# Performance work log

Hardware: AMD Instinct MI355X
Metric: run time of the kernel (lower is better)

Reference implementation:

```python
import jax, jax.numpy as jnp
import numpy as np

# dims (see shape_source)
B, S, N, F_IN = 8, 32, 512, 24   # batch, sections, nodes/section, node feat
C = 56                            # GAT out_channels (hidden_size)
EB, ES = 262144, 8192             # bend edges (over S*N nodes), section edges (over N nodes)
ED = 4                            # edge_dim
NEG_SLOPE_ATT = 0.2               # GATConv leaky_relu slope


def setup_inputs() -> dict:
    key = jax.random.key(0)
    ks = jax.random.split(key, 24)
    sd = 0.1
    inp = {}
    inp["x"] = jax.random.normal(ks[0], (B, S, N, F_IN), jnp.float32)
    inp["bend_edge_index"] = jax.random.randint(ks[1], (2, EB), 0, S * N)
    inp["section_edge_index"] = jax.random.randint(ks[2], (2, ES), 0, N)
    inp["bend_edge_attr"] = jax.random.normal(ks[3], (B, EB, ED), jnp.float32)
    inp["section_edge_attr"] = jax.random.normal(ks[4], (B, ES, ED), jnp.float32)
    # edge encoder Linear(4, 4)
    inp["enc_W"] = jax.random.normal(ks[5], (ED, ED), jnp.float32) * sd
    inp["enc_b"] = jax.random.normal(ks[6], (ED,), jnp.float32) * sd
    # GAT (bend) params: heads=1, concat=False
    inp["Wb"] = jax.random.normal(ks[7], (F_IN, C), jnp.float32) * sd
    inp["a_src_b"] = jax.random.normal(ks[8], (C,), jnp.float32) * sd
    inp["a_dst_b"] = jax.random.normal(ks[9], (C,), jnp.float32) * sd
    inp["We_b"] = jax.random.normal(ks[10], (ED, C), jnp.float32) * sd
    inp["a_e_b"] = jax.random.normal(ks[11], (C,), jnp.float32) * sd
    inp["bias_b"] = jax.random.normal(ks[12], (C,), jnp.float32) * sd
    # GAT (section) params
    inp["Ws"] = jax.random.normal(ks[13], (F_IN, C), jnp.float32) * sd
    inp["a_src_s"] = jax.random.normal(ks[14], (C,), jnp.float32) * sd
    inp["a_dst_s"] = jax.random.normal(ks[15], (C,), jnp.float32) * sd
    inp["We_s"] = jax.random.normal(ks[16], (ED, C), jnp.float32) * sd
    inp["a_e_s"] = jax.random.normal(ks[17], (C,), jnp.float32) * sd
    inp["bias_s"] = jax.random.normal(ks[18], (C,), jnp.float32) * sd
    # learnable mixing weights (nn.Parameter(torch.ones(2)))
    inp["mix_w"] = jnp.ones((2,), jnp.float32)
    return inp


def _segment_softmax(logits, seg, num_segments):
    m = jax.ops.segment_max(logits, seg, num_segments=num_segments)
    ex = jnp.exp(logits - m[seg])
    s = jax.ops.segment_sum(ex, seg, num_segments=num_segments)
    return ex / (s[seg] + 1e-16)


def _gat(x, edge_index, e_attr, W, a_src, a_dst, We, a_e, bias, num_nodes):
    """PyG GATConv (heads=1, concat=False, edge_dim) in eval mode on one graph."""
    h = x @ W                              # [Nn, C]
    e = e_attr @ We                        # [E, C] (lin_edge has no bias)
    src, dst = edge_index[0], edge_index[1]
    alpha_src = h @ a_src                  # [Nn]
    alpha_dst = h @ a_dst                  # [Nn]
    logits = jax.nn.leaky_relu(alpha_src[src] + alpha_dst[dst] + e @ a_e,
                               NEG_SLOPE_ATT)           # [E]
    att = _segment_softmax(logits, dst, num_nodes)      # softmax over incoming edges
    out = jax.ops.segment_sum(att[:, None] * h[src], dst, num_segments=num_nodes)
    return out + bias


def reference(x, bend_edge_index, section_edge_index, bend_edge_attr,
              section_edge_attr, enc_W, enc_b, Wb, a_src_b, a_dst_b, We_b,
              a_e_b, bias_b, Ws, a_src_s, a_dst_s, We_s, a_e_s, bias_s, mix_w):
    b, s, n, f = x.shape
    enc_bend = bend_edge_attr @ enc_W + enc_b       # [B, EB, ED]
    enc_sec = section_edge_attr @ enc_W + enc_b     # [B, ES, ED]

    # --- bend graph: one big graph of S*N nodes per sample, vmapped over batch
    x_flat = x.reshape(b, s * n, f)
    gat_bend = jax.vmap(lambda xi, ei: _gat(xi, bend_edge_index, ei, Wb,
                                            a_src_b, a_dst_b, We_b, a_e_b,
                                            bias_b, s * n))
    x_b_out = jax.nn.leaky_relu(gat_bend(x_flat, enc_bend), 0.01)  # [B, S*N, C]

    # --- section graphs: N-node graph per (sample, section); edge attrs shared
    # across sections within a sample (per the original loop).
    x_sec = x.reshape(b * s, n, f)
    enc_sec_rep = jnp.broadcast_to(enc_sec[:, None], (b, s) + enc_sec.shape[1:])
    enc_sec_rep = enc_sec_rep.reshape(b * s, enc_sec.shape[1], enc_sec.shape[2])
    gat_sec = jax.vmap(lambda xi, ei: _gat(xi, section_edge_index, ei, Ws,
                                           a_src_s, a_dst_s, We_s, a_e_s,
                                           bias_s, n))
    x_s_out = gat_sec(x_sec, enc_sec_rep).reshape(b, s * n, -1)    # [B, S*N, C]

    w = jax.nn.softmax(mix_w)
    return w[0] * x_b_out + w[1] * x_s_out
```

## Files before the change

### kernel.cpp

```cpp
#include <hip/hip_runtime.h>
#include <hip/hip_fp16.h>
#include <math.h>

#define BB 8
#define SS 32
#define NN 512
#define FIN 24
#define CC 56
#define EBN 262144
#define ESN 8192
#define EDD 4
#define NG (SS*NN)
#define BCAP 128
#define SCAP 128
#define HROW (CC*2)

__device__ __forceinline__ float wave_sum(float v) {
    #pragma unroll
    for (int o = 32; o > 0; o >>= 1) v += __shfl_xor(v, o);
    return v;
}

__global__ void k0_init(const float* enc_W, const float* enc_b,
                        const float* Wb, const float* a_src_b, const float* a_dst_b,
                        const float* We_b, const float* a_e_b,
                        const float* Ws, const float* a_src_s, const float* a_dst_s,
                        const float* We_s, const float* a_e_s,
                        const float* mix_w, float* P, int* cnts) {
    int i = blockIdx.x * blockDim.x + threadIdx.x;
    if (i < NG + NN) cnts[i] = 0;
    if (blockIdx.x == 0) {
        int t = threadIdx.x;
        if (t < 96) {
            int v = t / FIN, f = t % FIN;
            const float* W = (v < 2) ? Wb : Ws;
            const float* a = (v == 0) ? a_src_b : (v == 1) ? a_dst_b
                           : (v == 2) ? a_src_s : a_dst_s;
            float d = 0.f;
            for (int c = 0; c < CC; ++c) d = fmaf(W[f*CC + c], a[c], d);
            P[16 + t] = d;
        }
        if (t == 0) {
            float tb[EDD], ts[EDD];
            for (int j = 0; j < EDD; ++j) {
                float vb = 0.f, vs = 0.f;
                for (int c = 0; c < CC; ++c) {
                    vb += We_b[j*CC + c] * a_e_b[c];
                    vs += We_s[j*CC + c] * a_e_s[c];
                }
                tb[j] = vb; ts[j] = vs;
            }
            float cb = 0.f, cs = 0.f;
            for (int j = 0; j < EDD; ++j) { cb += enc_b[j]*tb[j]; cs += enc_b[j]*ts[j]; }
            for (int d = 0; d < EDD; ++d) {
                float ub = 0.f, us = 0.f;
                for (int j = 0; j < EDD; ++j) {
                    ub += enc_W[d*EDD + j] * tb[j];
                    us += enc_W[d*EDD + j] * ts[j];
                }
                P[d] = ub; P[5 + d] = us;
            }
            P[4] = cb; P[9] = cs;
            float m0 = mix_w[0], m1 = mix_w[1];
            float mm = fmaxf(m0, m1);
            float e0 = expf(m0 - mm), e1 = expf(m1 - mm);
            float inv = 1.f / (e0 + e1);
            P[10] = e0 * inv; P[11] = e1 * inv;
        }
    }
}

#define FNB 64
#define FEAT_NB (BB*NG/FNB)
#define FILLB_NB ((EBN+255)/256)
#define FILLS_NB ((ESN+255)/256)

__global__ __launch_bounds__(256, 4) void k1_all(
        const float* __restrict__ x,
        const int* __restrict__ bend_ei, const int* __restrict__ sec_ei,
        const float* __restrict__ bend_attr, const float* __restrict__ sec_attr,
        const float* __restrict__ Wb, const float* __restrict__ Ws,
        const float* __restrict__ P,
        unsigned short* __restrict__ h_b, unsigned short* __restrict__ h_s,
        float* __restrict__ asb, float* __restrict__ adb,
        float* __restrict__ ass, float* __restrict__ ads,
        int* __restrict__ bcnt, int* __restrict__ bbuck, float* __restrict__ elb_csr,
        int* __restrict__ scnt, int* __restrict__ sbuck, float* __restrict__ els_csr) {
    __shared__ float xs[FNB * FIN];
    int blk = blockIdx.x;
    int t = threadIdx.x;
    if (blk < FEAT_NB) {
        const float4* xg = (const float4*)(x + (size_t)blk * FNB * FIN);
        float4* xs4 = (float4*)xs;
        #pragma unroll
        for (int i = 0; i < (FNB*FIN/4 + 255) / 256; ++i) {
            int idx = t + i * 256;
            if (idx < FNB*FIN/4) xs4[idx] = xg[idx];
        }
        int w = t >> 6, lane = t & 63;
        int nl0 = w * (FNB / 4);
        __syncthreads();
        #pragma unroll 1
        for (int m = 0; m < 2; ++m) {
            const float* W = m ? Ws : Wb;
            unsigned short* h = m ? h_s : h_b;
            float* asx = m ? ass : asb;
            float* adx = m ? ads : adb;
            float wc[FIN];
            #pragma unroll
            for (int f = 0; f < FIN; ++f) {
                float v = 0.f;
                if (lane < CC) v = W[f*CC + lane];
                else if (lane < 58) v = P[16 + m*48 + (lane - 56)*FIN + f];
                wc[f] = v;
            }
            #pragma unroll 2
            for (int n0 = 0; n0 < FNB / 4; ++n0) {
                int nl = nl0 + n0;
                size_t node = (size_t)blk * FNB + nl;
                const float4* xr = (const float4*)(xs + nl * FIN);
                float acc = 0.f;
                #pragma unroll
                for (int q = 0; q < FIN/4; ++q) {
                    float4 v = xr[q];
                    acc = fmaf(v.x, wc[4*q+0], acc);
                    acc = fmaf(v.y, wc[4*q+1], acc);
                    acc = fmaf(v.z, wc[4*q+2], acc);
                    acc = fmaf(v.w, wc[4*q+3], acc);
                }
                if (lane < CC) h[node*CC + lane] = __half_as_ushort(__float2half(acc));
                else if (lane == 56) asx[node] = acc;
                else if (lane == 57) adx[node] = acc;
            }
        }
    } else if (blk < FEAT_NB + FILLB_NB) {
        int i = (blk - FEAT_NB) * 256 + t;
        if (i < EBN) {
            int s = bend_ei[i];
            int d = bend_ei[EBN + i];
            int p = atomicAdd(&bcnt[d], 1);
            if (p < BCAP) {
                bbuck[d * BCAP + p] = s;
                size_t slot = (size_t)d * BCAP + p;
                #pragma unroll
                for (int b = 0; b < BB; ++b) {
                    float4 a = ((const float4*)bend_attr)[(size_t)b * EBN + i];
                    elb_csr[(size_t)b * (NG * BCAP) + slot] =
                        fmaf(a.x, P[0], fmaf(a.y, P[1], fmaf(a.z, P[2], fmaf(a.w, P[3], P[4]))));
                }
            }
        }
    } else {
        int i = (blk - FEAT_NB - FILLB_NB) * 256 + t;
        if (i < ESN) {
            int s = sec_ei[i];
            int d = sec_ei[ESN + i];
            int p = atomicAdd(&scnt[d], 1);
            if (p < SCAP) {
                sbuck[d * SCAP + p] = s;
                size_t slot = (size_t)d * SCAP + p;
                #pragma unroll
                for (int b = 0; b < BB; ++b) {
                    float4 a = ((const float4*)sec_attr)[(size_t)b * ESN + i];
                    els_csr[(size_t)b * (NN * SCAP) + slot] =
                        fmaf(a.x, P[5], fmaf(a.y, P[6], fmaf(a.z, P[7], fmaf(a.w, P[8], P[9]))));
                }
            }
        }
    }
}

__device__ __forceinline__ float accum_f16(const unsigned short* pArr,
                                           const unsigned int* oArr,
                                           int deg, const char* __restrict__ hB,
                                           unsigned int cl2,
                                           unsigned int& psum2) {
    float a0 = 0.f, a1 = 0.f;
    const uint4* pv = (const uint4*)pArr;
    const uint4* ov = (const uint4*)oArr;
    int ng8 = (deg + 7) >> 3;
    for (int j = 0; j < ng8; ++j) {
        uint4 pq = pv[j];
        uint4 oa = ov[2*j];
        uint4 ob = ov[2*j+1];
        unsigned int h0 = *(const unsigned short*)(hB + (oa.x + cl2));
        unsigned int h1 = *(const unsigned short*)(hB + (oa.y + cl2));
        unsigned int h2 = *(const unsigned short*)(hB + (oa.z + cl2));
        unsigned int h3 = *(const unsigned short*)(hB + (oa.w + cl2));
        unsigned int h4 = *(const unsigned short*)(hB + (ob.x + cl2));
        unsigned int h5 = *(const unsigned short*)(hB + (ob.y + cl2));
        unsigned int h6 = *(const unsigned short*)(hB + (ob.z + cl2));
        unsigned int h7 = *(const unsigned short*)(hB + (ob.w + cl2));
        asm("v_pk_add_f16 %0, %0, %1" : "+v"(psum2) : "v"(pq.x));
        asm("v_pk_add_f16 %0, %0, %1" : "+v"(psum2) : "v"(pq.y));
        asm("v_pk_add_f16 %0, %0, %1" : "+v"(psum2) : "v"(pq.z));
        asm("v_pk_add_f16 %0, %0, %1" : "+v"(psum2) : "v"(pq.w));
        asm("v_fma_mix_f32 %0, %1, %2, %0 op_sel:[0,0,0] op_sel_hi:[1,1,0]" : "+v"(a0) : "v"(pq.x), "v"(h0));
        asm("v_fma_mix_f32 %0, %1, %2, %0 op_sel:[1,0,0] op_sel_hi:[1,1,0]" : "+v"(a1) : "v"(pq.x), "v"(h1));
        asm("v_fma_mix_f32 %0, %1, %2, %0 op_sel:[0,0,0] op_sel_hi:[1,1,0]" : "+v"(a0) : "v"(pq.y), "v"(h2));
        asm("v_fma_mix_f32 %0, %1, %2, %0 op_sel:[1,0,0] op_sel_hi:[1,1,0]" : "+v"(a1) : "v"(pq.y), "v"(h3));
        asm("v_fma_mix_f32 %0, %1, %2, %0 op_sel:[0,0,0] op_sel_hi:[1,1,0]" : "+v"(a0) : "v"(pq.z), "v"(h4));
        asm("v_fma_mix_f32 %0, %1, %2, %0 op_sel:[1,0,0] op_sel_hi:[1,1,0]" : "+v"(a1) : "v"(pq.z), "v"(h5));
        asm("v_fma_mix_f32 %0, %1, %2, %0 op_sel:[0,0,0] op_sel_hi:[1,1,0]" : "+v"(a0) : "v"(pq.w), "v"(h6));
        asm("v_fma_mix_f32 %0, %1, %2, %0 op_sel:[1,0,0] op_sel_hi:[1,1,0]" : "+v"(a1) : "v"(pq.w), "v"(h7));
    }
    return a0 + a1;
}

__device__ __noinline__ float gat_big(const int* __restrict__ buck,
                                      const float* __restrict__ elc, int deg,
                                      const float* __restrict__ asrc,
                                      const char* __restrict__ hB,
                                      float adg, int lane, unsigned int cl2,
                                      unsigned short* pArr, unsigned int* oArr) {
    if (deg <= 0) return 0.f;
    float acc = 0.f, sum = 0.f;
    for (int k0 = 0; k0 < deg; k0 += 64) {
        int k = k0 + lane;
        bool v = k < deg;
        unsigned idx = v ? (unsigned)k : 0u;
        unsigned s = (unsigned)buck[idx];
        float lg = asrc[s] + adg + elc[idx];
        lg = fmaxf(lg, 0.2f * lg);
        float p = v ? __expf(lg) : 0.f;
        asm volatile("s_waitcnt lgkmcnt(0)" ::: "memory");
        pArr[lane] = __half_as_ushort(__float2half(p));
        oArr[lane] = s * HROW;
        sum += wave_sum(p);
        asm volatile("s_waitcnt lgkmcnt(0)" ::: "memory");
        int valid = (deg - k0) < 64 ? (deg - k0) : 64;
        unsigned int dummy = 0;
        acc += accum_f16(pArr, oArr, valid, hB, cl2, dummy);
    }
    return acc * __builtin_amdgcn_rcpf(sum + 1e-16f);
}

__global__ __launch_bounds__(256, 8) void k2_gather(
        const int* __restrict__ bcnt, const int* __restrict__ bbuck,
        const float* __restrict__ elb_csr,
        const int* __restrict__ scnt, const int* __restrict__ sbuck,
        const float* __restrict__ els_csr,
        const unsigned short* __restrict__ h_b, const unsigned short* __restrict__ h_s,
        const float* __restrict__ asb, const float* __restrict__ adb,
        const float* __restrict__ ass, const float* __restrict__ ads,
        const float* __restrict__ bias_b, const float* __restrict__ bias_s,
        const float* __restrict__ P, float* __restrict__ out) {
    __shared__ __align__(16) unsigned short pLds[4][2][64];
    __shared__ __align__(16) unsigned int   oLds[4][2][64];
    int blk = blockIdx.x;
    int b = blk & 7;
    int w = threadIdx.x >> 6;
    unsigned int g = (((unsigned)blk >> 3) << 2) + w;
    unsigned int lane = threadIdx.x & 63;
    unsigned int cl2 = (lane < CC ? lane : 0) * 2;

    int degb = bcnt[g];  degb = degb < BCAP ? degb : BCAP;
    unsigned int sct = g >> 9;
    unsigned int n = g & (NN - 1);
    int degs = scnt[n];  degs = degs < SCAP ? degs : SCAP;

    const int* bb = bbuck + (size_t)g * BCAP;
    const float* elbp = elb_csr + (size_t)b * (NG * BCAP) + (size_t)g * BCAP;
    const int* sb = sbuck + (size_t)n * SCAP;
    const float* elsp = els_csr + (size_t)b * (NN * SCAP) + (size_t)n * SCAP;
    const float* asrcb = asb + (size_t)b * NG;
    const char* hbB = (const char*)(h_b + (size_t)b * NG * CC);
    size_t basebg = (size_t)b * NG + (size_t)sct * NN;
    const float* asrcs = ass + basebg;
    const char* hsB = (const char*)(h_s + basebg * CC);
    float adgb = adb[(size_t)b * NG + g];
    float adgs = ads[basebg + n];

    float vb, vs;
    if (degb <= 64 && degs <= 64) {
        bool vB = lane < (unsigned)degb, vS = lane < (unsigned)degs;
        unsigned slb = vB ? lane : 0u;
        unsigned sls = vS ? lane : 0u;
        unsigned srcb = (unsigned)bb[slb];
        unsigned srcs = (unsigned)sb[sls];
        float elbv = elbp[slb];
        float elsv = elsp[sls];
        float lgb = asrcb[srcb] + adgb + elbv;
        float lgs = asrcs[srcs] + adgs + elsv;
        lgb = fmaxf(lgb, 0.2f * lgb);
        lgs = fmaxf(lgs, 0.2f * lgs);
        float pb = vB ? __expf(lgb) : 0.f;
        float ps = vS ? __expf(lgs) : 0.f;
        pLds[w][0][lane] = __half_as_ushort(__float2half(pb));
        pLds[w][1][lane] = __half_as_ushort(__float2half(ps));
        oLds[w][0][lane] = srcb * HROW;
        oLds[w][1][lane] = srcs * HROW;
        asm volatile("s_waitcnt lgkmcnt(0)" ::: "memory");
        unsigned int psumb = 0u, psums = 0u;
        float accb = accum_f16(&pLds[w][0][0], &oLds[w][0][0], degb, hbB, cl2, psumb);
        float accs = accum_f16(&pLds[w][1][0], &oLds[w][1][0], degs, hsB, cl2, psums);
        __half2 hb2 = __builtin_bit_cast(__half2, psumb);
        __half2 hs2 = __builtin_bit_cast(__half2, psums);
        float sumb = __low2float(hb2) + __high2float(hb2);
        float sums = __low2float(hs2) + __high2float(hs2);
        vb = accb * __builtin_amdgcn_rcpf(sumb + 1e-16f);
        vs = accs * __builtin_amdgcn_rcpf(sums + 1e-16f);
    } else {
        vb = gat_big(bb, elbp, degb, asrcb, hbB, adgb, lane, cl2,
                     &pLds[w][0][0], &oLds[w][0][0]);
        vs = gat_big(sb, elsp, degs, asrcs, hsB, adgs, lane, cl2,
                     &pLds[w][1][0], &oLds[w][1][0]);
    }

    if (lane < CC) {
        float ob = vb + bias_b[lane];
        ob = fmaxf(ob, 0.01f * ob);
        float os = vs + bias_s[lane];
        out[((size_t)b * NG + g) * CC + lane] = P[10] * ob + P[11] * os;
    }
}

extern "C" void kernel_launch(void* const* d_in, const int* in_sizes, int n_in,
                              void* d_out, int out_size, void* d_ws, size_t ws_size,
                              hipStream_t stream) {
    const float* x          = (const float*)d_in[0];
    const int*   bend_ei    = (const int*)d_in[1];
    const int*   sec_ei     = (const int*)d_in[2];
    const float* bend_attr  = (const float*)d_in[3];
    const float* sec_attr   = (const float*)d_in[4];
    const float* enc_W      = (const float*)d_in[5];
    const float* enc_b      = (const float*)d_in[6];
    const float* Wb         = (const float*)d_in[7];
    const float* a_src_b    = (const float*)d_in[8];
    const float* a_dst_b    = (const float*)d_in[9];
    const float* We_b       = (const float*)d_in[10];
    const float* a_e_b      = (const float*)d_in[11];
    const float* bias_b     = (const float*)d_in[12];
    const float* Ws         = (const float*)d_in[13];
    const float* a_src_s    = (const float*)d_in[14];
    const float* a_dst_s    = (const float*)d_in[15];
    const float* We_s       = (const float*)d_in[16];
    const float* a_e_s      = (const float*)d_in[17];
    const float* bias_s     = (const float*)d_in[18];
    const float* mix_w      = (const float*)d_in[19];
    float* out = (float*)d_out;

    char* base = (char*)d_ws;
    size_t off = 0;
    auto alloc = [&](size_t bytes) -> char* {
        off = (off + 255) & ~(size_t)255;
        char* p = base + off;
        off += bytes;
        return p;
    };
    float* P        = (float*)alloc(128 * sizeof(float));
    int* bcnt       = (int*)alloc((NG + NN) * sizeof(int));
    int* scnt       = bcnt + NG;
    int* bbuck      = (int*)alloc((size_t)NG * BCAP * sizeof(int));
    int* sbuck      = (int*)alloc((size_t)NN * SCAP * sizeof(int));
    float* elb_csr  = (float*)alloc((size_t)BB * NG * BCAP * sizeof(float));
    float* els_csr  = (float*)alloc((size_t)BB * NN * SCAP * sizeof(float));
    unsigned short* h_b = (unsigned short*)alloc((size_t)BB * NG * CC * sizeof(unsigned short));
    unsigned short* h_s = (unsigned short*)alloc((size_t)BB * NG * CC * sizeof(unsigned short));
    float* asb      = (float*)alloc((size_t)BB * NG * sizeof(float));
    float* adb      = (float*)alloc((size_t)BB * NG * sizeof(float));
    float* ass      = (float*)alloc((size_t)BB * NG * sizeof(float));
    float* ads      = (float*)alloc((size_t)BB * NG * sizeof(float));
    (void)ws_size; (void)in_sizes; (void)n_in; (void)out_size;

    k0_init<<<(NG + NN + 255) / 256, 256, 0, stream>>>(enc_W, enc_b,
                                                       Wb, a_src_b, a_dst_b, We_b, a_e_b,
                                                       Ws, a_src_s, a_dst_s, We_s, a_e_s,
                                                       mix_w, P, bcnt);

    int k1_blocks = FEAT_NB + FILLB_NB + FILLS_NB;
    k1_all<<<k1_blocks, 256, 0, stream>>>(x, bend_ei, sec_ei, bend_attr, sec_attr,
                                          Wb, Ws, P, h_b, h_s, asb, adb, ass, ads,
                                          bcnt, bbuck, elb_csr, scnt, sbuck, els_csr);

    int k2_blocks = 8 * (NG / 4);
    k2_gather<<<k2_blocks, 256, 0, stream>>>(bcnt, bbuck, elb_csr, scnt, sbuck, els_csr,
                                             h_b, h_s, asb, adb, ass, ads,
                                             bias_b, bias_s, P, out);
}
```

Measured before the change: 139.7 us.

## Split edge logit computation from CSR fill via edge-id buckets and transpose kernel

Edge-attribute logits are now computed in a fully coalesced pass over the attribute arrays into an edge-ordered buffer. The bucket fill stores edge ids instead of doing eight strided attribute reads and scattered writes per edge. A new transpose kernel then gathers logits into the per-destination CSR layout, walking slots in order so the writes are coalesced. The aim is to replace scattered attribute traffic in the atomic fill, at the cost of an extra kernel launch, an extra intermediate buffer round-trip, and random gathers in the transpose.

After: 154.2 us. +10.4%, slower.

```diff
diff --git a/kernel.cpp b/kernel.cpp
--- a/kernel.cpp
+++ b/kernel.cpp
@@ -74,6 +74,7 @@
 #define FEAT_NB (BB*NG/FNB)
 #define FILLB_NB ((EBN+255)/256)
 #define FILLS_NB ((ESN+255)/256)
+#define ELOG_NB ((BB*(EBN+ESN)+255)/256)
 
 __global__ __launch_bounds__(256, 4) void k1_all(
         const float* __restrict__ x,
@@ -84,8 +85,9 @@
         unsigned short* __restrict__ h_b, unsigned short* __restrict__ h_s,
         float* __restrict__ asb, float* __restrict__ adb,
         float* __restrict__ ass, float* __restrict__ ads,
-        int* __restrict__ bcnt, int* __restrict__ bbuck, float* __restrict__ elb_csr,
-        int* __restrict__ scnt, int* __restrict__ sbuck, float* __restrict__ els_csr) {
+        float* __restrict__ elog_b, float* __restrict__ elog_s,
+        int* __restrict__ bcnt, int* __restrict__ bbuck, int* __restrict__ bbeid,
+        int* __restrict__ scnt, int* __restrict__ sbuck, int* __restrict__ sbeid) {
     __shared__ float xs[FNB * FIN];
     int blk = blockIdx.x;
     int t = threadIdx.x;
@@ -141,16 +143,10 @@
             int p = atomicAdd(&bcnt[d], 1);
             if (p < BCAP) {
                 bbuck[d * BCAP + p] = s;
-                size_t slot = (size_t)d * BCAP + p;
-                #pragma unroll
-                for (int b = 0; b < BB; ++b) {
-                    float4 a = ((const float4*)bend_attr)[(size_t)b * EBN + i];
-                    elb_csr[(size_t)b * (NG * BCAP) + slot] =
-                        fmaf(a.x, P[0], fmaf(a.y, P[1], fmaf(a.z, P[2], fmaf(a.w, P[3], P[4]))));
-                }
-            }
-        }
-    } else {
+                bbeid[d * BCAP + p] = i;
+            }
+        }
+    } else if (blk < FEAT_NB + FILLB_NB + FILLS_NB) {
         int i = (blk - FEAT_NB - FILLB_NB) * 256 + t;
         if (i < ESN) {
             int s = sec_ei[i];
@@ -158,13 +154,52 @@
             int p = atomicAdd(&scnt[d], 1);
             if (p < SCAP) {
                 sbuck[d * SCAP + p] = s;
-                size_t slot = (size_t)d * SCAP + p;
+                sbeid[d * SCAP + p] = i;
+            }
+        }
+    } else {
+        int i = (blk - FEAT_NB - FILLB_NB - FILLS_NB) * 256 + t;
+        const int nb = BB * EBN;
+        if (i < nb) {
+            float4 a = ((const float4*)bend_attr)[i];
+            elog_b[i] = fmaf(a.x, P[0], fmaf(a.y, P[1], fmaf(a.z, P[2], fmaf(a.w, P[3], P[4]))));
+        } else if (i < nb + BB * ESN) {
+            int j = i - nb;
+            float4 a = ((const float4*)sec_attr)[j];
+            elog_s[j] = fmaf(a.x, P[5], fmaf(a.y, P[6], fmaf(a.z, P[7], fmaf(a.w, P[8], P[9]))));
+        }
+    }
+}
+
+#define TSB_NB ((NG*BCAP + 255)/256)
+#define TSS_NB ((NN*SCAP + 255)/256)
+
+__global__ __launch_bounds__(256, 8) void kt_transpose(
+        const int* __restrict__ bcnt, const int* __restrict__ bbeid,
+        const float* __restrict__ elog_b, float* __restrict__ elb_csr,
+        const int* __restrict__ scnt, const int* __restrict__ sbeid,
+        const float* __restrict__ elog_s, float* __restrict__ els_csr) {
+    int blk = blockIdx.x;
+    if (blk < TSB_NB) {
+        unsigned slot = (unsigned)blk * 256 + threadIdx.x;
+        unsigned node = slot >> 7;
+        unsigned k = slot & (BCAP - 1);
+        if ((int)k < bcnt[node]) {
+            unsigned eid = (unsigned)bbeid[slot];
+            #pragma unroll
+            for (int b = 0; b < BB; ++b)
+                elb_csr[(size_t)b * (NG * BCAP) + slot] = elog_b[(size_t)b * EBN + eid];
+        }
+    } else {
+        unsigned slot = (unsigned)(blk - TSB_NB) * 256 + threadIdx.x;
+        if (slot < NN * SCAP) {
+            unsigned node = slot >> 7;
+            unsigned k = slot & (SCAP - 1);
+            if ((int)k < scnt[node]) {
+                unsigned eid = (unsigned)sbeid[slot];
                 #pragma unroll
-                for (int b = 0; b < BB; ++b) {
-                    float4 a = ((const float4*)sec_attr)[(size_t)b * ESN + i];
-                    els_csr[(size_t)b * (NN * SCAP) + slot] =
-                        fmaf(a.x, P[5], fmaf(a.y, P[6], fmaf(a.z, P[7], fmaf(a.w, P[8], P[9]))));
-                }
+                for (int b = 0; b < BB; ++b)
+                    els_csr[(size_t)b * (NN * SCAP) + slot] = elog_s[(size_t)b * ESN + eid];
             }
         }
     }
@@ -352,7 +387,11 @@
     int* bcnt       = (int*)alloc((NG + NN) * sizeof(int));
     int* scnt       = bcnt + NG;
     int* bbuck      = (int*)alloc((size_t)NG * BCAP * sizeof(int));
+    int* bbeid      = (int*)alloc((size_t)NG * BCAP * sizeof(int));
     int* sbuck      = (int*)alloc((size_t)NN * SCAP * sizeof(int));
+    int* sbeid      = (int*)alloc((size_t)NN * SCAP * sizeof(int));
+    float* elog_b   = (float*)alloc((size_t)BB * EBN * sizeof(float));
+    float* elog_s   = (float*)alloc((size_t)BB * ESN * sizeof(float));
     float* elb_csr  = (float*)alloc((size_t)BB * NG * BCAP * sizeof(float));
     float* els_csr  = (float*)alloc((size_t)BB * NN * SCAP * sizeof(float));
     unsigned short* h_b = (unsigned short*)alloc((size_t)BB * NG * CC * sizeof(unsigned short));
@@ -368,10 +407,14 @@
                                                        Ws, a_src_s, a_dst_s, We_s, a_e_s,
                                                        mix_w, P, bcnt);
 
-    int k1_blocks = FEAT_NB + FILLB_NB + FILLS_NB;
+    int k1_blocks = FEAT_NB + FILLB_NB + FILLS_NB + ELOG_NB;
     k1_all<<<k1_blocks, 256, 0, stream>>>(x, bend_ei, sec_ei, bend_attr, sec_attr,
                                           Wb, Ws, P, h_b, h_s, asb, adb, ass, ads,
-                                          bcnt, bbuck, elb_csr, scnt, sbuck, els_csr);
+                                          elog_b, elog_s,
+                                          bcnt, bbuck, bbeid, scnt, sbuck, sbeid);
+
+    kt_transpose<<<TSB_NB + TSS_NB, 256, 0, stream>>>(bcnt, bbeid, elog_b, elb_csr,
+                                                      scnt, sbeid, elog_s, els_csr);
 
     int k2_blocks = 8 * (NG / 4);
     k2_gather<<<k2_blocks, 256, 0, stream>>>(bcnt, bbuck, elb_csr, scnt, sbuck, els_csr,
```
